# Kernel tuning notes

Measured on AMD Instinct MI355X. Metric: run time of the kernel, lower is better.

## Reference

```python
import jax, jax.numpy as jnp
import numpy as np

MAX_DEG = 10
DEG_COUNTS = [10000, 130000, 170000, 160000, 100000, 15000, 5000, 2500, 2500, 2500, 2500]
DEG_STARTS = [int(s) for s in np.concatenate([[0], np.cumsum(DEG_COUNTS)[:-1]])]
N_ATOMS = int(sum(DEG_COUNTS))
BATCH = 24000
N_TASKS = 12
IN_FEAT = 75
CHANNELS = [IN_FEAT, 15, 20, 27, 36]


def setup_inputs() -> dict:
    key = jax.random.key(0)
    ks = jax.random.split(key, 32)
    inp = {}
    inp['atom_features'] = jax.random.normal(ks[0], (N_ATOMS, IN_FEAT), dtype=jnp.float32)
    # degree_slice[d] = (start, count) of atoms of degree d (atoms are sorted by degree)
    inp['degree_slice'] = jnp.array(np.stack([DEG_STARTS, DEG_COUNTS], axis=1), dtype=jnp.int32)
    inp['membership'] = jax.random.randint(ks[1], (N_ATOMS,), 0, BATCH, dtype=jnp.int32)
    for d in range(1, MAX_DEG + 1):
        inp[f'deg_adj_{d}'] = jax.random.randint(ks[1 + d], (DEG_COUNTS[d], d), 0, N_ATOMS, dtype=jnp.int32)
    for i in range(4):
        fi, fo = CHANNELS[i], CHANNELS[i + 1]
        inp[f'W{i+1}'] = (jax.random.normal(ks[12 + 2 * i], (2 * MAX_DEG + 1, fi, fo), dtype=jnp.float32)
                          / np.float32(np.sqrt(fi)))
        inp[f'b{i+1}'] = jnp.zeros((2 * MAX_DEG + 1, fo), dtype=jnp.float32)
    inp['W_dense'] = jax.random.normal(ks[30], (2 * CHANNELS[-1], N_TASKS * 2), dtype=jnp.float32) / np.float32(np.sqrt(2 * CHANNELS[-1]))
    inp['b_dense'] = jnp.zeros((N_TASKS * 2,), dtype=jnp.float32)
    return inp


def graph_conv(atoms, deg_adjs, W, b):
    # W: [2*MAX_DEG+1, in, out]; weight iterator order: (rel_d, self_d) for d=1..MAX_DEG, then self_0
    outs = [None] * (MAX_DEG + 1)
    for deg in range(1, MAX_DEG + 1):
        adj = deg_adjs[deg - 1]                      # [n_d, deg] neighbor indices
        rel = jnp.sum(atoms[adj], axis=1)            # gather + sum over neighbors -> [n_d, in]
        s, c = DEG_STARTS[deg], DEG_COUNTS[deg]
        self_atoms = atoms[s:s + c]                  # atoms of this degree (static slice)
        i = 2 * (deg - 1)
        outs[deg] = (rel @ W[i] + b[i]) + (self_atoms @ W[i + 1] + b[i + 1])
    outs[0] = atoms[:DEG_COUNTS[0]] @ W[2 * MAX_DEG] + b[2 * MAX_DEG]
    return jax.nn.selu(jnp.concatenate(outs, axis=0))


def graph_gather(atoms, membership):
    sums = jax.ops.segment_sum(atoms, membership, num_segments=BATCH)
    maxs = jax.ops.segment_max(atoms, membership, num_segments=BATCH)
    return jnp.tanh(jnp.concatenate([sums, maxs], axis=1))  # [BATCH, 2*36]


def reference(atom_features, degree_slice, membership,
              deg_adj_1, deg_adj_2, deg_adj_3, deg_adj_4, deg_adj_5,
              deg_adj_6, deg_adj_7, deg_adj_8, deg_adj_9, deg_adj_10,
              W1, b1, W2, b2, W3, b3, W4, b4, W_dense, b_dense):
    # degree_slice carries the same (start,count) info as the static DEG_STARTS/DEG_COUNTS.
    deg_adjs = [deg_adj_1, deg_adj_2, deg_adj_3, deg_adj_4, deg_adj_5,
                deg_adj_6, deg_adj_7, deg_adj_8, deg_adj_9, deg_adj_10]
    x = graph_conv(atom_features, deg_adjs, W1, b1)
    x = graph_conv(x, deg_adjs, W2, b2)
    x = graph_conv(x, deg_adjs, W3, b3)
    x = graph_conv(x, deg_adjs, W4, b4)
    mol = graph_gather(x, membership)                 # [BATCH, 72]
    logits = (mol @ W_dense + b_dense).reshape(BATCH, N_TASKS, 2)
    return jax.nn.softmax(logits, axis=-1)
```

## Files before the change

### kernel.cpp

```cpp
#include <hip/hip_runtime.h>
#include <hip/hip_fp16.h>
#include <cstdint>

#define NT 256
#define N_ATOMS_C 600000
#define BATCH_C 24000

constexpr int K_COUNTS[11] = {10000,130000,170000,160000,100000,15000,5000,2500,2500,2500,2500};
constexpr int K_STARTS[11] = {0,10000,140000,310000,470000,570000,585000,590000,592500,595000,597500};
constexpr int DORD[11] = {10,9,8,7,6,5,4,3,2,1,0};

struct AdjPtrs { const int* p[10]; };

__device__ __forceinline__ float selu_f(float x) {
    const float scale = 1.0507009873554805f;
    const float alpha = 1.6732632423543772f;
    return scale * (x > 0.f ? x : alpha * expm1f(x));
}

__device__ __forceinline__ float2 up2(unsigned u) {
    const __half2 h = __builtin_bit_cast(__half2, u);
    return __half22float2(h);
}
__device__ __forceinline__ unsigned pack2(float a, float b) {
    const __half2 h = __float22half2_rn(make_float2(a, b));
    return __builtin_bit_cast(unsigned, h);
}

template<int NLD4>
__device__ __forceinline__ void load_row(const uint2* __restrict__ p, float* r) {
#pragma unroll
    for (int v = 0; v < NLD4; ++v) {
        const uint2 t = p[v];
        const float2 a = up2(t.x), b = up2(t.y);
        r[4*v] = a.x; r[4*v+1] = a.y; r[4*v+2] = b.x; r[4*v+3] = b.y;
    }
}
template<int NLD4>
__device__ __forceinline__ void add_row(const uint2* __restrict__ p, float* r) {
#pragma unroll
    for (int v = 0; v < NLD4; ++v) {
        const uint2 t = p[v];
        const float2 a = up2(t.x), b = up2(t.y);
        r[4*v] += a.x; r[4*v+1] += a.y; r[4*v+2] += b.x; r[4*v+3] += b.y;
    }
}
template<int NF, int FO>
__device__ __forceinline__ void fma_strip(const float* r, const float* __restrict__ w,
                                          float* acc) {
#pragma unroll
    for (int f = 0; f < NF; ++f)
#pragma unroll
        for (int o = 0; o < FO; ++o)
            acc[o] = fmaf(r[f], w[f * FO + o], acc[o]);
}

template<int FIN, int FINP, int FO, int FOP, int FS, bool OUTF32>
__global__ __launch_bounds__(256) void conv_kernel(
    const unsigned short* __restrict__ x,
    const float* __restrict__ W,
    const float* __restrict__ bias,
    AdjPtrs adjp,
    void* __restrict__ yv)
{
    static_assert(FS % 4 == 0 && FINP % 4 == 0, "");
    constexpr int NSF = FIN / FS;
    constexpr int TF  = FIN - NSF * FS;
    constexpr int TLD4 = (TF + 3) / 4;
    static_assert(NSF * FS + TLD4 * 4 <= FINP, "tail reads past row");

    int blk = blockIdx.x;
    int deg = 0, s = 0, cnt = 0;
#pragma unroll
    for (int di = 0; di < 11; ++di) {
        const int d = DORD[di];
        const int nb = (K_COUNTS[d] + NT - 1) / NT;
        if (blk < nb) { deg = d; s = K_STARTS[d]; cnt = K_COUNTS[d]; break; }
        blk -= nb;
    }
    const int a = blk * NT + threadIdx.x;
    if (a >= cnt) return;
    const int atom = s + a;

    const int wi_a = (deg == 0) ? 20 : 2 * (deg - 1);
    const int wi_b = (deg == 0) ? 20 : 2 * deg - 1;
    const float* Wa = W + wi_a * FIN * FO;
    const float* Wb = W + wi_b * FIN * FO;

    float acc[FO];
#pragma unroll
    for (int o = 0; o < FO; ++o)
        acc[o] = bias[wi_b * FO + o] + ((deg > 0) ? bias[wi_a * FO + o] : 0.f);

    const int* myadj = (deg > 0) ? (adjp.p[deg - 1] + (size_t)a * deg) : nullptr;
    const uint2* selfrow = reinterpret_cast<const uint2*>(x + (size_t)atom * FINP);

#pragma unroll 1
    for (int st = 0; st < NSF; ++st) {
        const int f0 = st * FS;
        float r[FS];
        load_row<FS / 4>(selfrow + (f0 >> 2), r);
        fma_strip<FS, FO>(r, Wb + f0 * FO, acc);
        if (deg > 0) {
#pragma unroll
            for (int f = 0; f < FS; ++f) r[f] = 0.f;
            for (int k = 0; k < deg; ++k)
                add_row<FS / 4>(reinterpret_cast<const uint2*>(
                    x + (size_t)myadj[k] * FINP) + (f0 >> 2), r);
            fma_strip<FS, FO>(r, Wa + f0 * FO, acc);
        }
    }
    if constexpr (TF > 0) {
        constexpr int f0 = NSF * FS;
        float r[TLD4 * 4];
        load_row<TLD4>(selfrow + (f0 >> 2), r);
        fma_strip<TF, FO>(r, Wb + f0 * FO, acc);
        if (deg > 0) {
#pragma unroll
            for (int f = 0; f < TLD4 * 4; ++f) r[f] = 0.f;
            for (int k = 0; k < deg; ++k)
                add_row<TLD4>(reinterpret_cast<const uint2*>(
                    x + (size_t)myadj[k] * FINP) + (f0 >> 2), r);
            fma_strip<TF, FO>(r, Wa + f0 * FO, acc);
        }
    }

    float outv[FOP];
#pragma unroll
    for (int o = 0; o < FOP; ++o) outv[o] = (o < FO) ? selu_f(acc[o]) : 0.f;

    if constexpr (OUTF32) {
        float4* yp = reinterpret_cast<float4*>((float*)yv + (size_t)atom * FOP);
#pragma unroll
        for (int v = 0; v < FOP / 4; ++v)
            yp[v] = make_float4(outv[4*v], outv[4*v+1], outv[4*v+2], outv[4*v+3]);
    } else {
        uint2* yp = reinterpret_cast<uint2*>((unsigned short*)yv + (size_t)atom * FOP);
#pragma unroll
        for (int v = 0; v < FOP / 4; ++v)
            yp[v] = make_uint2(pack2(outv[4*v], outv[4*v+1]),
                               pack2(outv[4*v+2], outv[4*v+3]));
    }
}

__global__ __launch_bounds__(256) void cast_kernel(const float* __restrict__ x0,
                                                   unsigned short* __restrict__ xh)
{
    const int i = blockIdx.x * NT + threadIdx.x;
    if (i >= N_ATOMS_C * 19) return;
    const int atom = i / 19, v = i - atom * 19;
    const int f0 = v * 4;
    float t[4];
#pragma unroll
    for (int j = 0; j < 4; ++j)
        t[j] = (f0 + j < 75) ? x0[(size_t)atom * 75 + f0 + j] : 0.f;
    reinterpret_cast<uint2*>(xh)[i] = make_uint2(pack2(t[0], t[1]), pack2(t[2], t[3]));
}

__global__ __launch_bounds__(256) void zero_cnt_kernel(int* __restrict__ cnt) {
    const int i = blockIdx.x * NT + threadIdx.x;
    if (i < BATCH_C) cnt[i] = 0;
}
__global__ __launch_bounds__(256) void count_kernel(const int* __restrict__ mem,
                                                    int* __restrict__ cnt) {
    const int i = blockIdx.x * NT + threadIdx.x;
    if (i < N_ATOMS_C) atomicAdd(&cnt[mem[i]], 1);
}
__global__ __launch_bounds__(1024) void scan_kernel(const int* __restrict__ cnt,
                                                    int* __restrict__ base,
                                                    int* __restrict__ cursor) {
    __shared__ int part[1024];
    const int tid = threadIdx.x;
    constexpr int CH = 24;
    const int i0 = tid * CH;
    int sum = 0;
    for (int j = 0; j < CH; ++j) { const int i = i0 + j; if (i < BATCH_C) sum += cnt[i]; }
    part[tid] = sum;
    __syncthreads();
    for (int off = 1; off < 1024; off <<= 1) {
        const int v = (tid >= off) ? part[tid - off] : 0;
        __syncthreads(); part[tid] += v; __syncthreads();
    }
    int run = part[tid] - sum;
    for (int j = 0; j < CH; ++j) {
        const int i = i0 + j;
        if (i < BATCH_C) { base[i] = run; cursor[i] = run; run += cnt[i]; }
    }
    if (tid == 1023) base[BATCH_C] = part[1023];
}
__global__ __launch_bounds__(256) void scatter_kernel(const int* __restrict__ mem,
                                                      int* __restrict__ cursor,
                                                      int* __restrict__ alist) {
    const int i = blockIdx.x * NT + threadIdx.x;
    if (i < N_ATOMS_C) { const int p = atomicAdd(&cursor[mem[i]], 1); alist[p] = i; }
}

__global__ __launch_bounds__(256) void reduce_dense_kernel(
    const unsigned short* __restrict__ y4,
    const int* __restrict__ base, const int* __restrict__ alist,
    const float* __restrict__ Wd, const float* __restrict__ bd,
    float* __restrict__ out)
{
    __shared__ float sW[72 * 24];
    __shared__ float sb[24];
    __shared__ float molf[4][72];

    const int tid = threadIdx.x;
    for (int i = tid; i < 72 * 24; i += NT) sW[i] = Wd[i];
    if (tid < 24) sb[tid] = bd[tid];
    __syncthreads();

    const int w = tid >> 6, lane = tid & 63;
    const int mol = blockIdx.x * 4 + w;
    const int b0 = base[mol], b1 = base[mol + 1];

    if (lane < 36) {
        float s = 0.f, mx = -INFINITY;
        for (int k = b0; k < b1; ++k) {
            const int atom = alist[k];
            const float v = __half2float(__builtin_bit_cast(__half,
                                y4[(size_t)atom * 36 + lane]));
            s += v; mx = fmaxf(mx, v);
        }
        molf[w][lane] = tanhf(s);
        molf[w][36 + lane] = tanhf(mx);
    }
    __syncthreads();

    if (lane < 24) {
        float l = sb[lane];
#pragma unroll
        for (int f = 0; f < 72; ++f) l += molf[w][f] * sW[f * 24 + lane];
        const float lp = __shfl_xor(l, 1);
        const float m2 = fmaxf(l, lp);
        const float e = expf(l - m2), ep = expf(lp - m2);
        out[(size_t)mol * 24 + lane] = e / (e + ep);
    }
}

extern "C" void kernel_launch(void* const* d_in, const int* in_sizes, int n_in,
                              void* d_out, int out_size, void* d_ws, size_t ws_size,
                              hipStream_t stream)
{
    const float* x0         = (const float*)d_in[0];
    const int*   membership = (const int*)d_in[2];
    AdjPtrs adj;
    for (int d = 0; d < 10; ++d) adj.p[d] = (const int*)d_in[3 + d];
    const float *W1=(const float*)d_in[13], *b1=(const float*)d_in[14];
    const float *W2=(const float*)d_in[15], *b2=(const float*)d_in[16];
    const float *W3=(const float*)d_in[17], *b3=(const float*)d_in[18];
    const float *W4=(const float*)d_in[19], *b4=(const float*)d_in[20];
    const float *Wd=(const float*)d_in[21], *bd=(const float*)d_in[22];

    const size_t szA = (size_t)N_ATOMS_C * 76 * 2;
    const size_t szB = (size_t)N_ATOMS_C * 28 * 2;
    const size_t szC = (size_t)N_ATOMS_C * 20 * 2;
    const size_t nInts = (size_t)N_ATOMS_C + (BATCH_C + 1) + BATCH_C + BATCH_C;
    if (ws_size < szA + szB + szC + nInts * 4) return;

    unsigned short* xh  = (unsigned short*)d_ws;
    unsigned short* y4  = (unsigned short*)d_ws;
    unsigned short* y13 = (unsigned short*)((char*)d_ws + szA);
    unsigned short* y2  = (unsigned short*)((char*)d_ws + szA + szB);
    int* alist  = (int*)((char*)d_ws + szA + szB + szC);
    int* base   = alist + N_ATOMS_C;
    int* cursor = base + (BATCH_C + 1);
    int* cnt    = cursor + BATCH_C;

    int nblk = 0;
    for (int d = 0; d < 11; ++d) nblk += (K_COUNTS[d] + NT - 1) / NT;
    const int nb_atoms = (N_ATOMS_C + NT - 1) / NT;

    cast_kernel<<<(N_ATOMS_C * 19 + NT - 1) / NT, NT, 0, stream>>>(x0, xh);

    zero_cnt_kernel<<<(BATCH_C + NT - 1) / NT, NT, 0, stream>>>(cnt);
    count_kernel<<<nb_atoms, NT, 0, stream>>>(membership, cnt);
    scan_kernel<<<1, 1024, 0, stream>>>(cnt, base, cursor);
    scatter_kernel<<<nb_atoms, NT, 0, stream>>>(membership, cursor, alist);

    conv_kernel<75,76,15,16,76,false><<<nblk, NT, 0, stream>>>(xh,  W1, b1, adj, y13);
    conv_kernel<15,16,20,20,16,false><<<nblk, NT, 0, stream>>>(y13, W2, b2, adj, y2);
    conv_kernel<20,20,27,28,20,false><<<nblk, NT, 0, stream>>>(y2,  W3, b3, adj, y13);
    conv_kernel<27,28,36,36,28,false><<<nblk, NT, 0, stream>>>(y13, W4, b4, adj, y4);

    reduce_dense_kernel<<<BATCH_C / 4, NT, 0, stream>>>(y4, base, alist, Wd, bd, (float*)d_out);
}
```

Measured before the change: 619.1 us.

## Precompute per-atom projections for layer 1 so low-degree gathers read narrow rows

Result: slower. 699.3 us (+13.0%).

```diff
diff --git a/kernel.cpp b/kernel.cpp
--- a/kernel.cpp
+++ b/kernel.cpp
@@ -55,31 +55,178 @@
             acc[o] = fmaf(r[f], w[f * FO + o], acc[o]);
 }
 
-template<int FIN, int FINP, int FO, int FOP, int FS, bool OUTF32>
+__device__ __forceinline__ void blk2deg(int blk, int& deg, int& s, int& cnt, int& tile) {
+    deg = 0; s = 0; cnt = 0; tile = 0;
+#pragma unroll
+    for (int di = 0; di < 11; ++di) {
+        const int d = DORD[di];
+        const int nb = (K_COUNTS[d] + NT - 1) / NT;
+        if (blk < nb) { deg = d; s = K_STARTS[d]; cnt = K_COUNTS[d]; tile = blk; return; }
+        blk -= nb;
+    }
+}
+
+__global__ __launch_bounds__(256) void prep_kernel(
+    const float* __restrict__ x0,
+    const float* __restrict__ W,
+    const float* __restrict__ bias,
+    const int* __restrict__ mem,
+    int* __restrict__ cnt,
+    unsigned short* __restrict__ z,
+    unsigned short* __restrict__ srow)
+{
+    int deg, s, c, tile;
+    blk2deg(blockIdx.x, deg, s, c, tile);
+    const int a = tile * NT + threadIdx.x;
+    if (a >= c) return;
+    const int atom = s + a;
+
+    const int wi_b = deg ? (2 * deg - 1) : 20;
+    const float* Wz0 = W;
+    const float* Wz1 = W + 2 * 1125;
+    const float* Wz2 = W + 4 * 1125;
+    const float* Wz3 = W + 6 * 1125;
+    const float* Wsb = W + wi_b * 1125;
+
+    float z0[15], z1[15], z2[15], z3[15], sa[15];
+#pragma unroll
+    for (int o = 0; o < 15; ++o) {
+        z0[o] = 0.f; z1[o] = 0.f; z2[o] = 0.f; z3[o] = 0.f;
+        sa[o] = bias[wi_b * 15 + o] + (deg ? bias[2 * (deg - 1) * 15 + o] : 0.f);
+    }
+
+    const float* xr = x0 + (size_t)atom * 75;
+#pragma unroll 1
+    for (int st = 0; st < 5; ++st) {
+        float r[15];
+#pragma unroll
+        for (int j = 0; j < 15; ++j) r[j] = xr[st * 15 + j];
+#pragma unroll
+        for (int f = 0; f < 15; ++f) {
+            const float rv = r[f];
+            const int fg = st * 15 + f;
+#pragma unroll
+            for (int o = 0; o < 15; ++o) {
+                z0[o] = fmaf(rv, Wz0[fg * 15 + o], z0[o]);
+                z1[o] = fmaf(rv, Wz1[fg * 15 + o], z1[o]);
+                z2[o] = fmaf(rv, Wz2[fg * 15 + o], z2[o]);
+                z3[o] = fmaf(rv, Wz3[fg * 15 + o], z3[o]);
+                sa[o] = fmaf(rv, Wsb[fg * 15 + o], sa[o]);
+            }
+        }
+    }
+
+    uint2* zp = reinterpret_cast<uint2*>(z + (size_t)atom * 64);
+#define ZW(P, arr) \
+    zp[P*4+0] = make_uint2(pack2(arr[0],arr[1]),  pack2(arr[2],arr[3]));   \
+    zp[P*4+1] = make_uint2(pack2(arr[4],arr[5]),  pack2(arr[6],arr[7]));   \
+    zp[P*4+2] = make_uint2(pack2(arr[8],arr[9]),  pack2(arr[10],arr[11])); \
+    zp[P*4+3] = make_uint2(pack2(arr[12],arr[13]),pack2(arr[14],0.f));
+    ZW(0, z0) ZW(1, z1) ZW(2, z2) ZW(3, z3)
+#undef ZW
+    uint2* sp = reinterpret_cast<uint2*>(srow + (size_t)atom * 16);
+    sp[0] = make_uint2(pack2(sa[0],sa[1]),  pack2(sa[2],sa[3]));
+    sp[1] = make_uint2(pack2(sa[4],sa[5]),  pack2(sa[6],sa[7]));
+    sp[2] = make_uint2(pack2(sa[8],sa[9]),  pack2(sa[10],sa[11]));
+    sp[3] = make_uint2(pack2(sa[12],sa[13]),pack2(sa[14],0.f));
+
+    atomicAdd(&cnt[mem[atom]], 1);
+}
+
+__global__ __launch_bounds__(256) void conv1_kernel(
+    const float* __restrict__ x0,
+    const unsigned short* __restrict__ z,
+    const unsigned short* __restrict__ srow,
+    const float* __restrict__ W,
+    AdjPtrs adjp,
+    unsigned short* __restrict__ y1)
+{
+    int deg, s, c, tile;
+    blk2deg(blockIdx.x, deg, s, c, tile);
+    const int a = tile * NT + threadIdx.x;
+    if (a >= c) return;
+    const int atom = s + a;
+
+    float acc[15];
+    {
+        const uint2* sp = reinterpret_cast<const uint2*>(srow + (size_t)atom * 16);
+        float r[16];
+        load_row<4>(sp, r);
+#pragma unroll
+        for (int o = 0; o < 15; ++o) acc[o] = r[o];
+    }
+
+    if (deg >= 1 && deg <= 4) {
+        const int* ad = adjp.p[deg - 1] + (size_t)a * deg;
+        int nb[4];
+#pragma unroll
+        for (int k = 0; k < 4; ++k) nb[k] = ad[k < deg ? k : 0];
+        uint2 t[4][4];
+#pragma unroll
+        for (int k = 0; k < 4; ++k) {
+            const uint2* p = reinterpret_cast<const uint2*>(
+                z + (size_t)nb[k] * 64 + (deg - 1) * 16);
+#pragma unroll
+            for (int v = 0; v < 4; ++v) t[k][v] = p[v];
+        }
+#pragma unroll
+        for (int k = 0; k < 4; ++k) {
+            if (k < deg) {
+                float r[16];
+#pragma unroll
+                for (int v = 0; v < 4; ++v) {
+                    const float2 lo = up2(t[k][v].x), hi = up2(t[k][v].y);
+                    r[4*v] = lo.x; r[4*v+1] = lo.y; r[4*v+2] = hi.x; r[4*v+3] = hi.y;
+                }
+#pragma unroll
+                for (int o = 0; o < 15; ++o) acc[o] += r[o];
+            }
+        }
+    } else if (deg >= 5) {
+        const float* Wa = W + 2 * (deg - 1) * 1125;
+        const int* ad = adjp.p[deg - 1] + (size_t)a * deg;
+#pragma unroll 1
+        for (int st = 0; st < 3; ++st) {
+            float r[25];
+#pragma unroll
+            for (int j = 0; j < 25; ++j) r[j] = 0.f;
+            for (int k = 0; k < deg; ++k) {
+                const float* xr = x0 + (size_t)ad[k] * 75 + st * 25;
+#pragma unroll
+                for (int j = 0; j < 25; ++j) r[j] += xr[j];
+            }
+            fma_strip<25, 15>(r, Wa + st * 25 * 15, acc);
+        }
+    }
+
+    uint2* yp = reinterpret_cast<uint2*>(y1 + (size_t)atom * 16);
+    float o_[16];
+#pragma unroll
+    for (int o = 0; o < 16; ++o) o_[o] = (o < 15) ? selu_f(acc[o]) : 0.f;
+    yp[0] = make_uint2(pack2(o_[0],o_[1]),  pack2(o_[2],o_[3]));
+    yp[1] = make_uint2(pack2(o_[4],o_[5]),  pack2(o_[6],o_[7]));
+    yp[2] = make_uint2(pack2(o_[8],o_[9]),  pack2(o_[10],o_[11]));
+    yp[3] = make_uint2(pack2(o_[12],o_[13]),pack2(o_[14],o_[15]));
+}
+
+template<int FIN, int FINP, int FO, int FOP, int FS>
 __global__ __launch_bounds__(256) void conv_kernel(
     const unsigned short* __restrict__ x,
     const float* __restrict__ W,
     const float* __restrict__ bias,
     AdjPtrs adjp,
-    void* __restrict__ yv)
+    unsigned short* __restrict__ y)
 {
-    static_assert(FS % 4 == 0 && FINP % 4 == 0, "");
+    static_assert(FS % 4 == 0 && FINP % 4 == 0 && FOP % 4 == 0, "");
     constexpr int NSF = FIN / FS;
     constexpr int TF  = FIN - NSF * FS;
     constexpr int TLD4 = (TF + 3) / 4;
     static_assert(NSF * FS + TLD4 * 4 <= FINP, "tail reads past row");
 
-    int blk = blockIdx.x;
-    int deg = 0, s = 0, cnt = 0;
-#pragma unroll
-    for (int di = 0; di < 11; ++di) {
-        const int d = DORD[di];
-        const int nb = (K_COUNTS[d] + NT - 1) / NT;
-        if (blk < nb) { deg = d; s = K_STARTS[d]; cnt = K_COUNTS[d]; break; }
-        blk -= nb;
-    }
-    const int a = blk * NT + threadIdx.x;
-    if (a >= cnt) return;
+    int deg, s, c, tile;
+    blk2deg(blockIdx.x, deg, s, c, tile);
+    const int a = tile * NT + threadIdx.x;
+    if (a >= c) return;
     const int atom = s + a;
 
     const int wi_a = (deg == 0) ? 20 : 2 * (deg - 1);
@@ -128,43 +275,16 @@
     float outv[FOP];
 #pragma unroll
     for (int o = 0; o < FOP; ++o) outv[o] = (o < FO) ? selu_f(acc[o]) : 0.f;
-
-    if constexpr (OUTF32) {
-        float4* yp = reinterpret_cast<float4*>((float*)yv + (size_t)atom * FOP);
-#pragma unroll
-        for (int v = 0; v < FOP / 4; ++v)
-            yp[v] = make_float4(outv[4*v], outv[4*v+1], outv[4*v+2], outv[4*v+3]);
-    } else {
-        uint2* yp = reinterpret_cast<uint2*>((unsigned short*)yv + (size_t)atom * FOP);
-#pragma unroll
-        for (int v = 0; v < FOP / 4; ++v)
-            yp[v] = make_uint2(pack2(outv[4*v], outv[4*v+1]),
-                               pack2(outv[4*v+2], outv[4*v+3]));
-    }
-}
-
-__global__ __launch_bounds__(256) void cast_kernel(const float* __restrict__ x0,
-                                                   unsigned short* __restrict__ xh)
-{
-    const int i = blockIdx.x * NT + threadIdx.x;
-    if (i >= N_ATOMS_C * 19) return;
-    const int atom = i / 19, v = i - atom * 19;
-    const int f0 = v * 4;
-    float t[4];
-#pragma unroll
-    for (int j = 0; j < 4; ++j)
-        t[j] = (f0 + j < 75) ? x0[(size_t)atom * 75 + f0 + j] : 0.f;
-    reinterpret_cast<uint2*>(xh)[i] = make_uint2(pack2(t[0], t[1]), pack2(t[2], t[3]));
+    uint2* yp = reinterpret_cast<uint2*>(y + (size_t)atom * FOP);
+#pragma unroll
+    for (int v = 0; v < FOP / 4; ++v)
+        yp[v] = make_uint2(pack2(outv[4*v], outv[4*v+1]),
+                           pack2(outv[4*v+2], outv[4*v+3]));
 }
 
 __global__ __launch_bounds__(256) void zero_cnt_kernel(int* __restrict__ cnt) {
     const int i = blockIdx.x * NT + threadIdx.x;
     if (i < BATCH_C) cnt[i] = 0;
-}
-__global__ __launch_bounds__(256) void count_kernel(const int* __restrict__ mem,
-                                                    int* __restrict__ cnt) {
-    const int i = blockIdx.x * NT + threadIdx.x;
-    if (i < N_ATOMS_C) atomicAdd(&cnt[mem[i]], 1);
 }
 __global__ __launch_bounds__(1024) void scan_kernel(const int* __restrict__ cnt,
                                                     int* __restrict__ base,
@@ -252,17 +372,19 @@
     const float *W4=(const float*)d_in[19], *b4=(const float*)d_in[20];
     const float *Wd=(const float*)d_in[21], *bd=(const float*)d_in[22];
 
-    const size_t szA = (size_t)N_ATOMS_C * 76 * 2;
-    const size_t szB = (size_t)N_ATOMS_C * 28 * 2;
-    const size_t szC = (size_t)N_ATOMS_C * 20 * 2;
+    const size_t szA = 81600000;
+    const size_t szB = 38400000;
     const size_t nInts = (size_t)N_ATOMS_C + (BATCH_C + 1) + BATCH_C + BATCH_C;
-    if (ws_size < szA + szB + szC + nInts * 4) return;
-
-    unsigned short* xh  = (unsigned short*)d_ws;
-    unsigned short* y4  = (unsigned short*)d_ws;
-    unsigned short* y13 = (unsigned short*)((char*)d_ws + szA);
-    unsigned short* y2  = (unsigned short*)((char*)d_ws + szA + szB);
-    int* alist  = (int*)((char*)d_ws + szA + szB + szC);
+    if (ws_size < szA + szB + nInts * 4) return;
+
+    char* base0 = (char*)d_ws;
+    unsigned short* zbuf = (unsigned short*)base0;
+    unsigned short* y2   = (unsigned short*)base0;
+    unsigned short* y4   = (unsigned short*)(base0 + 38400000);
+    unsigned short* srow = (unsigned short*)(base0 + szA);
+    unsigned short* y1   = (unsigned short*)(base0 + szA + 9600000);
+    unsigned short* y3   = (unsigned short*)(base0 + szA);
+    int* alist  = (int*)(base0 + szA + szB);
     int* base   = alist + N_ATOMS_C;
     int* cursor = base + (BATCH_C + 1);
     int* cnt    = cursor + BATCH_C;
@@ -271,17 +393,15 @@
     for (int d = 0; d < 11; ++d) nblk += (K_COUNTS[d] + NT - 1) / NT;
     const int nb_atoms = (N_ATOMS_C + NT - 1) / NT;
 
-    cast_kernel<<<(N_ATOMS_C * 19 + NT - 1) / NT, NT, 0, stream>>>(x0, xh);
-
     zero_cnt_kernel<<<(BATCH_C + NT - 1) / NT, NT, 0, stream>>>(cnt);
-    count_kernel<<<nb_atoms, NT, 0, stream>>>(membership, cnt);
+    prep_kernel<<<nblk, NT, 0, stream>>>(x0, W1, b1, membership, cnt, zbuf, srow);
     scan_kernel<<<1, 1024, 0, stream>>>(cnt, base, cursor);
     scatter_kernel<<<nb_atoms, NT, 0, stream>>>(membership, cursor, alist);
 
-    conv_kernel<75,76,15,16,76,false><<<nblk, NT, 0, stream>>>(xh,  W1, b1, adj, y13);
-    conv_kernel<15,16,20,20,16,false><<<nblk, NT, 0, stream>>>(y13, W2, b2, adj, y2);
-    conv_kernel<20,20,27,28,20,false><<<nblk, NT, 0, stream>>>(y2,  W3, b3, adj, y13);
-    conv_kernel<27,28,36,36,28,false><<<nblk, NT, 0, stream>>>(y13, W4, b4, adj, y4);
+    conv1_kernel<<<nblk, NT, 0, stream>>>(x0, zbuf, srow, W1, adj, y1);
+    conv_kernel<15,16,20,32,16><<<nblk, NT, 0, stream>>>(y1, W2, b2, adj, y2);
+    conv_kernel<20,32,27,32,32><<<nblk, NT, 0, stream>>>(y2, W3, b3, adj, y3);
+    conv_kernel<27,32,36,36,32><<<nblk, NT, 0, stream>>>(y3, W4, b4, adj, y4);
 
     reduce_dense_kernel<<<BATCH_C / 4, NT, 0, stream>>>(y4, base, alist, Wd, bd, (float*)d_out);
 }
```
